# Optimization experiments

Hardware: AMD Instinct MI355X
Metric: run time of the kernel (lower is better)

The kernel has to match this reference:

```python
import jax, jax.numpy as jnp
import numpy as np

DIM = 1024
N_HEADS = 16
HEAD_DIM = DIM // N_HEADS


def setup_inputs() -> dict:
    key = jax.random.key(0)
    k_x, k_qkv_w, k_qkv_b, k_p_w, k_p_b = jax.random.split(key, 5)
    s = 1.0 / np.sqrt(DIM)
    return {
        "x": jax.random.normal(k_x, (2, 2048, DIM), dtype=jnp.float32),
        # stored as [in, out] so forward is x @ W + b (equivalent to torch Linear)
        "qkv_w": jax.random.uniform(k_qkv_w, (DIM, 3 * DIM), minval=-s, maxval=s, dtype=jnp.float32),
        "qkv_b": jax.random.uniform(k_qkv_b, (3 * DIM,), minval=-s, maxval=s, dtype=jnp.float32),
        "proj_w": jax.random.uniform(k_p_w, (DIM, DIM), minval=-s, maxval=s, dtype=jnp.float32),
        "proj_b": jax.random.uniform(k_p_b, (DIM,), minval=-s, maxval=s, dtype=jnp.float32),
    }


def reference(x, qkv_w, qkv_b, proj_w, proj_b):
    b, s, _ = x.shape
    qkv = x @ qkv_w + qkv_b                       # [b, s, 3*dim]
    q, k, v = jnp.split(qkv, 3, axis=-1)
    def split_heads(t):
        return t.reshape(b, s, N_HEADS, HEAD_DIM).transpose(0, 2, 1, 3)  # [b, h, s, d]
    q, k, v = map(split_heads, (q, k, v))
    scale = 1.0 / np.sqrt(HEAD_DIM)
    scores = jnp.einsum("bhqd,bhkd->bhqk", q, k) * scale
    attn = jax.nn.softmax(scores, axis=-1)
    out = jnp.einsum("bhqk,bhkd->bhqd", attn, v)
    out = out.transpose(0, 2, 1, 3).reshape(b, s, DIM)
    return out @ proj_w + proj_b
```

## Files before the change

### kernel.cpp

```cpp
#include <hip/hip_runtime.h>
#include <hip/hip_bf16.h>

typedef __attribute__((ext_vector_type(8))) short bf16x8;
typedef __attribute__((ext_vector_type(4))) float f32x4;
typedef __attribute__((ext_vector_type(16))) float f32x16;
typedef __attribute__((ext_vector_type(4))) unsigned short u16x4;
typedef __attribute__((ext_vector_type(8))) unsigned short u16x8v;

#define S_LEN 2048
#define NHEAD 16
#define HDIM 64
#define DIM 1024

__device__ __forceinline__ unsigned short f2bf(float f) {
    union { float f; unsigned u; } x; x.f = f;
    unsigned r = x.u + 0x7FFFu + ((x.u >> 16) & 1u);
    return (unsigned short)(r >> 16);
}
__device__ __forceinline__ unsigned short f2bf_fast(float f) {
    union { float f; unsigned u; } x; x.f = f;
    return (unsigned short)((x.u + 0x8000u) >> 16);
}

__device__ __forceinline__ f32x4 mfma16(bf16x8 a, bf16x8 b, f32x4 c) {
    return __builtin_amdgcn_mfma_f32_16x16x32_bf16(a, b, c, 0, 0, 0);
}
__device__ __forceinline__ f32x16 mfma32(bf16x8 a, bf16x8 b, f32x16 c) {
    return __builtin_amdgcn_mfma_f32_32x32x16_bf16(a, b, c, 0, 0, 0);
}

__device__ __forceinline__ float fexp2(float x) {
#if __has_builtin(__builtin_amdgcn_exp2f)
    return __builtin_amdgcn_exp2f(x);
#else
    return exp2f(x);
#endif
}

__device__ __forceinline__ void gl_lds16(const void* g, void* l) {
    __builtin_amdgcn_global_load_lds(
        (const __attribute__((address_space(1))) unsigned int*)g,
        (__attribute__((address_space(3))) unsigned int*)l, 16, 0, 0);
}

__global__ __launch_bounds__(256) void xconv_kernel(const float* __restrict__ X,
                                                    unsigned short* __restrict__ Xb) {
    size_t i = ((size_t)blockIdx.x * 256 + threadIdx.x) * 8;
    float4 a = *reinterpret_cast<const float4*>(&X[i]);
    float4 b = *reinterpret_cast<const float4*>(&X[i + 4]);
    u16x8v o;
    o[0] = f2bf(a.x); o[1] = f2bf(a.y); o[2] = f2bf(a.z); o[3] = f2bf(a.w);
    o[4] = f2bf(b.x); o[5] = f2bf(b.y); o[6] = f2bf(b.z); o[7] = f2bf(b.w);
    *reinterpret_cast<u16x8v*>(&Xb[i]) = o;
}

__global__ __launch_bounds__(256) void wtrans_kernel(const float* __restrict__ W,
                                                     unsigned short* __restrict__ Wt,
                                                     int K, int N) {
    __shared__ float lds[64][65];
    int k0 = blockIdx.x * 64, n0 = blockIdx.y * 64;
    int tid = threadIdx.x;
    for (int idx = tid; idx < 1024; idx += 256) {
        int row = idx >> 4, c = (idx & 15) << 2;
        float4 v = *reinterpret_cast<const float4*>(&W[(size_t)(k0 + row) * N + n0 + c]);
        lds[row][c] = v.x; lds[row][c + 1] = v.y; lds[row][c + 2] = v.z; lds[row][c + 3] = v.w;
    }
    __syncthreads();
    for (int idx = tid; idx < 1024; idx += 256) {
        int row = idx >> 4, c = (idx & 15) << 2;
        u16x4 o;
        o[0] = f2bf(lds[c][row]);     o[1] = f2bf(lds[c + 1][row]);
        o[2] = f2bf(lds[c + 2][row]); o[3] = f2bf(lds[c + 3][row]);
        *reinterpret_cast<u16x4*>(&Wt[(size_t)(n0 + row) * K + k0 + c]) = o;
    }
}

template <int MODE>
__global__ __launch_bounds__(256) void gemm_kernel(
    const unsigned short* __restrict__ Ab, const unsigned short* __restrict__ Bt,
    const float* __restrict__ bias,
    unsigned short* __restrict__ Qb, unsigned short* __restrict__ Kb,
    unsigned short* __restrict__ Vt, float* __restrict__ outf) {
    __shared__ unsigned short Alds[128 * 64];
    __shared__ unsigned short Blds[128 * 64];
    const int tid = threadIdx.x;
    const int m0 = blockIdx.x * 128, n0 = blockIdx.y * 128;
    const int wid = tid >> 6, lane = tid & 63;
    const int wm = wid >> 1, wn = wid & 1;
    const int lr = lane & 15, lg = lane >> 4;

    const char* Abase = (const char*)(Ab + (size_t)m0 * 1024);
    const char* Bbase = (const char*)(Bt + (size_t)n0 * 1024);

    int srcOff[4], dstOff[4];
#pragma unroll
    for (int i = 0; i < 4; ++i) {
        int off = i * 4096 + wid * 1024 + lane * 16;
        int row = off >> 7, col = off & 127;
        srcOff[i] = row * 2048 + (col ^ ((row & 7) << 4));
        dstOff[i] = off;
    }
    const int swz = (lr & 7) << 4;

    f32x4 acc[4][4] = {};

    for (int kt = 0; kt < 16; ++kt) {
        __syncthreads();
#pragma unroll
        for (int i = 0; i < 4; ++i) {
            gl_lds16(Abase + srcOff[i] + kt * 128, (char*)Alds + dstOff[i]);
            gl_lds16(Bbase + srcOff[i] + kt * 128, (char*)Blds + dstOff[i]);
        }
        __syncthreads();

#pragma unroll
        for (int ks = 0; ks < 2; ++ks) {
            bf16x8 af[4], bfr[4];
#pragma unroll
            for (int i = 0; i < 4; ++i)
                af[i] = *reinterpret_cast<const bf16x8*>(
                    (const char*)Alds + (wm * 64 + i * 16 + lr) * 128 + ((ks * 64 + lg * 16) ^ swz));
#pragma unroll
            for (int j = 0; j < 4; ++j)
                bfr[j] = *reinterpret_cast<const bf16x8*>(
                    (const char*)Blds + (wn * 64 + j * 16 + lr) * 128 + ((ks * 64 + lg * 16) ^ swz));
            __builtin_amdgcn_s_setprio(1);
#pragma unroll
            for (int i = 0; i < 4; ++i)
#pragma unroll
                for (int j = 0; j < 4; ++j)
                    acc[i][j] = mfma16(af[i], bfr[j], acc[i][j]);
            __builtin_amdgcn_s_setprio(0);
        }
    }

    if constexpr (MODE == 0) {
        const int sec = n0 >> 10;
#pragma unroll
        for (int j = 0; j < 4; ++j) {
            int gn = n0 + wn * 64 + j * 16 + lr;
            float bv = bias[gn];
            int nn = gn & 1023, h = nn >> 6, d = nn & 63;
#pragma unroll
            for (int i = 0; i < 4; ++i) {
#pragma unroll
                for (int r = 0; r < 4; ++r) {
                    int m = m0 + wm * 64 + i * 16 + lg * 4 + r;
                    int b_ = m >> 11, s_ = m & 2047;
                    size_t bh = (size_t)(b_ * NHEAD + h);
                    float v = acc[i][j][r] + bv;
                    if (sec == 0)
                        Qb[(bh * S_LEN + s_) * HDIM + d] = f2bf(v * 0.18033688f);
                    else if (sec == 1)
                        Kb[(bh * S_LEN + s_) * HDIM + d] = f2bf(v);
                    else
                        Vt[(bh * HDIM + d) * S_LEN + s_] = f2bf(v);
                }
            }
        }
    } else {
#pragma unroll
        for (int j = 0; j < 4; ++j) {
            int gn = n0 + wn * 64 + j * 16 + lr;
            float bv = bias[gn];
#pragma unroll
            for (int i = 0; i < 4; ++i) {
#pragma unroll
                for (int r = 0; r < 4; ++r) {
                    int m = m0 + wm * 64 + i * 16 + lg * 4 + r;
                    outf[(size_t)m * DIM + gn] = acc[i][j][r] + bv;
                }
            }
        }
    }
}

#define NT (S_LEN / 64)
__global__ __launch_bounds__(256) void attn_kernel(const unsigned short* __restrict__ Qb,
                                                   const unsigned short* __restrict__ Kb,
                                                   const unsigned short* __restrict__ Vt,
                                                   unsigned short* __restrict__ Ob) {
    __shared__ unsigned short Klds[2][64 * 64];
    __shared__ unsigned short Vlds[2][64 * 64];
    const int L = blockIdx.x;
    const int xcd = L & 7, slot = L >> 3;
    const int bh = xcd + 8 * (slot & 3);
    const int qblk = slot >> 2;
    const int wid = threadIdx.x >> 6;
    const int lane = threadIdx.x & 63;
    const int l31 = lane & 31, hi = lane >> 5;
    const int q0 = qblk * 128 + wid * 32;

    const unsigned short* qrow = &Qb[((size_t)bh * S_LEN + q0 + l31) * HDIM];
    bf16x8 qf[4];
#pragma unroll
    for (int kst = 0; kst < 4; ++kst)
        qf[kst] = *reinterpret_cast<const bf16x8*>(&qrow[kst * 16 + hi * 8]);

    const char* kT = (const char*)&Kb[(size_t)bh * S_LEN * HDIM];
    const char* vT = (const char*)&Vt[(size_t)bh * HDIM * S_LEN];

    const int c0 = 2 * wid, c1 = 2 * wid + 1;
    const int ks0 = ((c0 >> 2) * 32 + l31) * 128 + (c0 & 3) * 32 + hi * 16;
    const int ks1 = ((c1 >> 2) * 32 + l31) * 128 + (c1 & 3) * 32 + hi * 16;
    const int vs0 = ((c0 >> 2) * 32 + l31) * 4096 + (c0 & 3) * 32 + hi * 16;
    const int vs1 = ((c1 >> 2) * 32 + l31) * 4096 + (c1 & 3) * 32 + hi * 16;
    const int du0 = c0 * 1024, du1 = c1 * 1024;

    float ls = 0.f;
    f32x16 acc[2] = {};

    gl_lds16(kT + ks0, (char*)Klds[0] + du0);
    gl_lds16(kT + ks1, (char*)Klds[0] + du1);
    gl_lds16(vT + vs0, (char*)Vlds[0] + du0);
    gl_lds16(vT + vs1, (char*)Vlds[0] + du1);
    __syncthreads();

    int cur = 0;
    for (int jt = 0; jt < NT; ++jt) {
        if (jt + 1 < NT) {
            char* kl = (char*)Klds[cur ^ 1]; char* vl = (char*)Vlds[cur ^ 1];
            size_t kof = (size_t)(jt + 1) * 8192, vof = (size_t)(jt + 1) * 128;
            gl_lds16(kT + kof + ks0, kl + du0);
            gl_lds16(kT + kof + ks1, kl + du1);
            gl_lds16(vT + vof + vs0, vl + du0);
            gl_lds16(vT + vof + vs1, vl + du1);
        }
        const char* kl = (const char*)Klds[cur] + lane * 16;
        const char* vl = (const char*)Vlds[cur] + lane * 16;

        f32x16 p[2] = {};
        __builtin_amdgcn_s_setprio(1);
#pragma unroll
        for (int ct = 0; ct < 2; ++ct)
#pragma unroll
            for (int kst = 0; kst < 4; ++kst) {
                bf16x8 kb = *reinterpret_cast<const bf16x8*>(kl + (ct * 4 + kst) * 1024);
                p[ct] = mfma32(kb, qf[kst], p[ct]);
            }
        __builtin_amdgcn_s_setprio(0);

#pragma unroll
        for (int ct = 0; ct < 2; ++ct)
#pragma unroll
            for (int r = 0; r < 16; ++r) {
                float e = fexp2(p[ct][r]);
                p[ct][r] = e;
                ls += e;
            }

        bf16x8 pa[4];
#pragma unroll
        for (int kst = 0; kst < 4; ++kst) {
            const int ctq = kst >> 1, rb = 8 * (kst & 1);
            unsigned aw[2], bw[2];
#pragma unroll
            for (int u = 0; u < 2; ++u) {
                unsigned a, b;
                asm("v_cvt_pk_bf16_f32 %0, %1, %2"
                    : "=v"(a) : "v"(p[ctq][rb + 2 * u]), "v"(p[ctq][rb + 2 * u + 1]));
                asm("v_cvt_pk_bf16_f32 %0, %1, %2"
                    : "=v"(b) : "v"(p[ctq][rb + 4 + 2 * u]), "v"(p[ctq][rb + 4 + 2 * u + 1]));
                asm volatile("v_permlane32_swap_b32 %0, %1" : "+v"(a), "+v"(b));
                aw[u] = a; bw[u] = b;
            }
            union { unsigned w[4]; bf16x8 v; } pu;
            pu.w[0] = aw[0]; pu.w[1] = aw[1]; pu.w[2] = bw[0]; pu.w[3] = bw[1];
            pa[kst] = pu.v;
        }

        __builtin_amdgcn_s_setprio(1);
#pragma unroll
        for (int dt = 0; dt < 2; ++dt)
#pragma unroll
            for (int kst = 0; kst < 4; ++kst) {
                bf16x8 vb = *reinterpret_cast<const bf16x8*>(vl + (dt * 4 + kst) * 1024);
                acc[dt] = mfma32(pa[kst], vb, acc[dt]);
            }
        __builtin_amdgcn_s_setprio(0);

        __syncthreads();
        cur ^= 1;
    }

    ls += __shfl_xor(ls, 32, 64);

    float inv[16];
#pragma unroll
    for (int r = 0; r < 16; ++r) {
        int rq = (r & 3) + 8 * (r >> 2) + 4 * hi;
        inv[r] = 1.f / __shfl(ls, rq, 64);
    }

    const int b_ = bh >> 4, h = bh & 15;
#pragma unroll
    for (int dt = 0; dt < 2; ++dt)
#pragma unroll
        for (int r = 0; r < 16; ++r) {
            int rq = (r & 3) + 8 * (r >> 2) + 4 * hi;
            float o = acc[dt][r] * inv[r];
            int q = q0 + rq;
            Ob[((size_t)(b_ * S_LEN + q)) * DIM + h * HDIM + dt * 32 + l31] = f2bf_fast(o);
        }
}

extern "C" void kernel_launch(void* const* d_in, const int* in_sizes, int n_in,
                              void* d_out, int out_size, void* d_ws, size_t ws_size,
                              hipStream_t stream) {
    const float* x      = (const float*)d_in[0];
    const float* qkv_w  = (const float*)d_in[1];
    const float* qkv_b  = (const float*)d_in[2];
    const float* proj_w = (const float*)d_in[3];
    const float* proj_b = (const float*)d_in[4];
    float* out = (float*)d_out;

    unsigned short* Wqkvt = (unsigned short*)d_ws;
    unsigned short* Wpt   = Wqkvt + 3072 * 1024;
    unsigned short* Qb    = Wpt + 1024 * 1024;
    unsigned short* Kb    = Qb + 32 * 2048 * 64;
    unsigned short* Vt    = Kb + 32 * 2048 * 64;
    unsigned short* Ob    = Vt + 32 * 2048 * 64;
    unsigned short* Xb    = Ob + 4096 * 1024;

    xconv_kernel<<<2048, 256, 0, stream>>>(x, Xb);
    wtrans_kernel<<<dim3(16, 48), 256, 0, stream>>>(qkv_w, Wqkvt, 1024, 3072);
    wtrans_kernel<<<dim3(16, 16), 256, 0, stream>>>(proj_w, Wpt, 1024, 1024);

    gemm_kernel<0><<<dim3(32, 24), 256, 0, stream>>>(Xb, Wqkvt, qkv_b, Qb, Kb, Vt, nullptr);
    attn_kernel<<<512, 256, 0, stream>>>(Qb, Kb, Vt, Ob);
    gemm_kernel<1><<<dim3(32, 8), 256, 0, stream>>>(Ob, Wpt, proj_b, nullptr, nullptr, nullptr, out);
}
```

Measured before the change: 121.9 us.

## Load K/V fragments straight to registers, dropping LDS staging and barriers

The attention kernel no longer stages K and V tiles through double-buffered shared memory with block-wide barriers. Each wave now loads its own K/V fragments from global memory into registers, using two register sets (A/B) as a ping-pong prefetch over 32-key steps. This removes LDS traffic and __syncthreads. The cost is that all four waves of a block, which share the same K/V, fetch it redundantly from global/L2, and the loads are now smaller per step. The s_setprio hints are also dropped.

```diff
diff --git a/kernel.cpp b/kernel.cpp
--- a/kernel.cpp
+++ b/kernel.cpp
@@ -175,13 +175,43 @@
     }
 }
 
-#define NT (S_LEN / 64)
+__device__ __forceinline__ void attn_step(const bf16x8 (&kr)[4], const bf16x8 (&vr)[4],
+                                          const bf16x8 (&qf)[4], float& ls, f32x16 (&acc)[2]) {
+    f32x16 p = {};
+#pragma unroll
+    for (int kst = 0; kst < 4; ++kst) p = mfma32(kr[kst], qf[kst], p);
+#pragma unroll
+    for (int r = 0; r < 16; ++r) { float e = fexp2(p[r]); p[r] = e; ls += e; }
+    bf16x8 pa[2];
+#pragma unroll
+    for (int k2 = 0; k2 < 2; ++k2) {
+        const int rb = 8 * k2;
+        unsigned aw[2], bw[2];
+#pragma unroll
+        for (int u = 0; u < 2; ++u) {
+            unsigned a, b;
+            asm("v_cvt_pk_bf16_f32 %0, %1, %2"
+                : "=v"(a) : "v"(p[rb + 2 * u]), "v"(p[rb + 2 * u + 1]));
+            asm("v_cvt_pk_bf16_f32 %0, %1, %2"
+                : "=v"(b) : "v"(p[rb + 4 + 2 * u]), "v"(p[rb + 4 + 2 * u + 1]));
+            asm volatile("v_permlane32_swap_b32 %0, %1" : "+v"(a), "+v"(b));
+            aw[u] = a; bw[u] = b;
+        }
+        union { unsigned w[4]; bf16x8 v; } pu;
+        pu.w[0] = aw[0]; pu.w[1] = aw[1]; pu.w[2] = bw[0]; pu.w[3] = bw[1];
+        pa[k2] = pu.v;
+    }
+#pragma unroll
+    for (int dt = 0; dt < 2; ++dt)
+#pragma unroll
+        for (int k2 = 0; k2 < 2; ++k2)
+            acc[dt] = mfma32(pa[k2], vr[dt * 2 + k2], acc[dt]);
+}
+
 __global__ __launch_bounds__(256) void attn_kernel(const unsigned short* __restrict__ Qb,
                                                    const unsigned short* __restrict__ Kb,
                                                    const unsigned short* __restrict__ Vt,
                                                    unsigned short* __restrict__ Ob) {
-    __shared__ unsigned short Klds[2][64 * 64];
-    __shared__ unsigned short Vlds[2][64 * 64];
     const int L = blockIdx.x;
     const int xcd = L & 7, slot = L >> 3;
     const int bh = xcd + 8 * (slot & 3);
@@ -200,87 +230,44 @@
     const char* kT = (const char*)&Kb[(size_t)bh * S_LEN * HDIM];
     const char* vT = (const char*)&Vt[(size_t)bh * HDIM * S_LEN];
 
-    const int c0 = 2 * wid, c1 = 2 * wid + 1;
-    const int ks0 = ((c0 >> 2) * 32 + l31) * 128 + (c0 & 3) * 32 + hi * 16;
-    const int ks1 = ((c1 >> 2) * 32 + l31) * 128 + (c1 & 3) * 32 + hi * 16;
-    const int vs0 = ((c0 >> 2) * 32 + l31) * 4096 + (c0 & 3) * 32 + hi * 16;
-    const int vs1 = ((c1 >> 2) * 32 + l31) * 4096 + (c1 & 3) * 32 + hi * 16;
-    const int du0 = c0 * 1024, du1 = c1 * 1024;
+    int kofs[4], vofs[4];
+#pragma unroll
+    for (int c = 0; c < 4; ++c) {
+        kofs[c] = l31 * 128 + c * 32 + hi * 16;
+        vofs[c] = ((c >> 1) * 32 + l31) * 4096 + (c & 1) * 32 + hi * 16;
+    }
 
     float ls = 0.f;
     f32x16 acc[2] = {};
 
-    gl_lds16(kT + ks0, (char*)Klds[0] + du0);
-    gl_lds16(kT + ks1, (char*)Klds[0] + du1);
-    gl_lds16(vT + vs0, (char*)Vlds[0] + du0);
-    gl_lds16(vT + vs1, (char*)Vlds[0] + du1);
-    __syncthreads();
-
-    int cur = 0;
-    for (int jt = 0; jt < NT; ++jt) {
-        if (jt + 1 < NT) {
-            char* kl = (char*)Klds[cur ^ 1]; char* vl = (char*)Vlds[cur ^ 1];
-            size_t kof = (size_t)(jt + 1) * 8192, vof = (size_t)(jt + 1) * 128;
-            gl_lds16(kT + kof + ks0, kl + du0);
-            gl_lds16(kT + kof + ks1, kl + du1);
-            gl_lds16(vT + vof + vs0, vl + du0);
-            gl_lds16(vT + vof + vs1, vl + du1);
-        }
-        const char* kl = (const char*)Klds[cur] + lane * 16;
-        const char* vl = (const char*)Vlds[cur] + lane * 16;
-
-        f32x16 p[2] = {};
-        __builtin_amdgcn_s_setprio(1);
-#pragma unroll
-        for (int ct = 0; ct < 2; ++ct)
-#pragma unroll
-            for (int kst = 0; kst < 4; ++kst) {
-                bf16x8 kb = *reinterpret_cast<const bf16x8*>(kl + (ct * 4 + kst) * 1024);
-                p[ct] = mfma32(kb, qf[kst], p[ct]);
+    bf16x8 kA[4], vA[4], kB[4], vB[4];
+#pragma unroll
+    for (int c = 0; c < 4; ++c) {
+        kA[c] = *reinterpret_cast<const bf16x8*>(kT + kofs[c]);
+        vA[c] = *reinterpret_cast<const bf16x8*>(vT + vofs[c]);
+    }
+
+    for (int jt = 0; jt < 64; jt += 2) {
+        {
+            const char* kp = kT + (jt + 1) * 4096;
+            const char* vp = vT + (jt + 1) * 64;
+#pragma unroll
+            for (int c = 0; c < 4; ++c) {
+                kB[c] = *reinterpret_cast<const bf16x8*>(kp + kofs[c]);
+                vB[c] = *reinterpret_cast<const bf16x8*>(vp + vofs[c]);
             }
-        __builtin_amdgcn_s_setprio(0);
-
-#pragma unroll
-        for (int ct = 0; ct < 2; ++ct)
-#pragma unroll
-            for (int r = 0; r < 16; ++r) {
-                float e = fexp2(p[ct][r]);
-                p[ct][r] = e;
-                ls += e;
+        }
+        attn_step(kA, vA, qf, ls, acc);
+        if (jt + 2 < 64) {
+            const char* kp = kT + (jt + 2) * 4096;
+            const char* vp = vT + (jt + 2) * 64;
+#pragma unroll
+            for (int c = 0; c < 4; ++c) {
+                kA[c] = *reinterpret_cast<const bf16x8*>(kp + kofs[c]);
+                vA[c] = *reinterpret_cast<const bf16x8*>(vp + vofs[c]);
             }
-
-        bf16x8 pa[4];
-#pragma unroll
-        for (int kst = 0; kst < 4; ++kst) {
-            const int ctq = kst >> 1, rb = 8 * (kst & 1);
-            unsigned aw[2], bw[2];
-#pragma unroll
-            for (int u = 0; u < 2; ++u) {
-                unsigned a, b;
-                asm("v_cvt_pk_bf16_f32 %0, %1, %2"
-                    : "=v"(a) : "v"(p[ctq][rb + 2 * u]), "v"(p[ctq][rb + 2 * u + 1]));
-                asm("v_cvt_pk_bf16_f32 %0, %1, %2"
-                    : "=v"(b) : "v"(p[ctq][rb + 4 + 2 * u]), "v"(p[ctq][rb + 4 + 2 * u + 1]));
-                asm volatile("v_permlane32_swap_b32 %0, %1" : "+v"(a), "+v"(b));
-                aw[u] = a; bw[u] = b;
-            }
-            union { unsigned w[4]; bf16x8 v; } pu;
-            pu.w[0] = aw[0]; pu.w[1] = aw[1]; pu.w[2] = bw[0]; pu.w[3] = bw[1];
-            pa[kst] = pu.v;
-        }
-
-        __builtin_amdgcn_s_setprio(1);
-#pragma unroll
-        for (int dt = 0; dt < 2; ++dt)
-#pragma unroll
-            for (int kst = 0; kst < 4; ++kst) {
-                bf16x8 vb = *reinterpret_cast<const bf16x8*>(vl + (dt * 4 + kst) * 1024);
-                acc[dt] = mfma32(pa[kst], vb, acc[dt]);
-            }
-        __builtin_amdgcn_s_setprio(0);
-
-        __syncthreads();
-        cur ^= 1;
+        }
+        attn_step(kB, vB, qf, ls, acc);
     }
 
     ls += __shfl_xor(ls, 32, 64);
```

Result: slower. 186.7 us (+53.2%).
